# Kernel optimization log

Hardware: AMD Instinct MI355X
Metric: run time of the kernel (lower is better)

The kernel has to match this reference:

```python
import jax, jax.numpy as jnp
import numpy as np

HIDDEN = 768
KV_DIM = HIDDEN // 3  # 256
BATCH, SEQ = 2, 8192
THETA = 10000.0


def rope_table(seq_len, dim):
    # Matches LlamaRotaryEmbedding: returns [1, seq_len, dim] sinusoid table
    pos = jnp.arange(seq_len, dtype=jnp.float32)                       # [S]
    freqs = THETA ** (-jnp.arange(0, dim, 2, dtype=jnp.float32) / dim)  # [dim/2]
    ang = pos[:, None] * freqs[None, :]                                 # [S, dim/2]
    return jnp.concatenate([jnp.sin(ang), jnp.cos(ang)], axis=-1)[None]  # [1, S, dim]


def setup_inputs() -> dict:
    key = jax.random.key(0)
    kx, kq, kk, kv, ko = jax.random.split(key, 5)
    s = 1.0 / np.sqrt(HIDDEN)
    return {
        "x": jax.random.normal(kx, (BATCH, SEQ, HIDDEN), dtype=jnp.float32),
        # torch nn.Linear weights: [out_features, in_features], y = x @ W.T
        "Wq": jax.random.uniform(kq, (HIDDEN, HIDDEN), jnp.float32, -s, s),
        "Wk": jax.random.uniform(kk, (KV_DIM, HIDDEN), jnp.float32, -s, s),
        "Wv": jax.random.uniform(kv, (KV_DIM, HIDDEN), jnp.float32, -s, s),
        "Wo": jax.random.uniform(ko, (HIDDEN, KV_DIM), jnp.float32, -s, s),
    }


def reference(x, Wq, Wk, Wv, Wo):
    B, S, H = x.shape
    # q/k projections are computed in the original but immediately OVERWRITTEN
    # by the rope table (the rope module ignores its input values). Kept here
    # for faithfulness; XLA will DCE them in forward.
    q = jnp.einsum('bsh,oh->bso', x, Wq)
    k = jnp.einsum('bsh,oh->bso', x, Wk)
    v = jnp.einsum('bsh,oh->bso', x, Wv)                # [B, S, KV_DIM]
    r = rope_table(S, H)                                 # [1, S, H] -> q == k == r
    attn_weights = jnp.matmul(r, jnp.swapaxes(r, -2, -1))  # [1, S, S]
    attn_probs = jax.nn.softmax(attn_weights, axis=-1)      # [1, S, S]
    attn_output = jnp.matmul(attn_probs, v)                 # broadcast -> [B, S, KV_DIM]
    out = jnp.einsum('bsk,ok->bso', attn_output, Wo)        # [B, S, H]
    return out
```

## Files before the change

### kernel.cpp

```cpp
#include <hip/hip_runtime.h>


typedef unsigned short u16;
typedef __attribute__((ext_vector_type(8))) short short8;
typedef __attribute__((ext_vector_type(4))) float float4v;

__device__ inline u16 f32_to_bf16(float f) {
  union { float f; unsigned int u; } v; v.f = f;
  unsigned int r = v.u + 0x7FFF + ((v.u >> 16) & 1);
  return (u16)(r >> 16);
}

__global__ __launch_bounds__(256)
void prep_weights(const float* __restrict__ Wv, const float* __restrict__ Wo,
                  u16* __restrict__ wvt, u16* __restrict__ wot) {
  int id = blockIdx.x * 256 + threadIdx.x;
  union { u16 h[4]; uint2 u; } p;
  if (id < 49152) {
    int e = id * 4, n = e / 768, k = e - n * 768;
    float4v v = *(const float4v*)(Wv + (size_t)n * 768 + k);
    p.h[0] = f32_to_bf16(v[0]); p.h[1] = f32_to_bf16(v[1]);
    p.h[2] = f32_to_bf16(v[2]); p.h[3] = f32_to_bf16(v[3]);
    int t = k >> 5, kk = k & 31;
    *(uint2*)(wvt + ((t * 256 + n) * 32 + kk)) = p.u;
  } else {
    int e = (id - 49152) * 4, n = e / 256, k = e - n * 256;
    float4v v = *(const float4v*)(Wo + (size_t)n * 256 + k);
    p.h[0] = f32_to_bf16(v[0]); p.h[1] = f32_to_bf16(v[1]);
    p.h[2] = f32_to_bf16(v[2]); p.h[3] = f32_to_bf16(v[3]);
    int t = k >> 5, kk = k & 31;
    *(uint2*)(wot + ((t * 768 + n) * 32 + kk)) = p.u;
  }
}

template <bool WS>
__global__ __launch_bounds__(512, 1)
void fused_mfma(const float* __restrict__ x,
                const float* __restrict__ Wv, const float* __restrict__ Wo,
                const u16* __restrict__ wvt, const u16* __restrict__ wot,
                float* __restrict__ out) {
  __shared__ __align__(16) u16 As[64 * 32];
  __shared__ __align__(16) u16 Bs[256 * 32];
  __shared__ __align__(16) u16 Vs[64 * 264];

  const int tid = threadIdx.x;
  const int w  = tid >> 6, l = tid & 63;
  const int q  = l >> 4, mr = l & 15;
  const int wm = w & 1, wn = w >> 1;
  const int row0 = blockIdx.x * 64;

  const int xr = tid >> 3, xg = (tid & 7) * 4;
  const int wr = tid >> 1, wh = (tid & 1) * 16;

  float4v acc[2][4];
#pragma unroll
  for (int i = 0; i < 2; ++i)
#pragma unroll
    for (int j = 0; j < 4; ++j) acc[i][j] = (float4v){0.f, 0.f, 0.f, 0.f};

  for (int kt = 0; kt < 24; ++kt) {
    const int k0 = kt * 32;
    {
      float4v v = *(const float4v*)(x + (size_t)(row0 + xr) * 768 + k0 + xg);
      union { u16 h[4]; uint2 u; } p;
      p.h[0] = f32_to_bf16(v[0]); p.h[1] = f32_to_bf16(v[1]);
      p.h[2] = f32_to_bf16(v[2]); p.h[3] = f32_to_bf16(v[3]);
      *(uint2*)(As + xr * 32 + xg) = p.u;
    }
    if (WS) {
      const u16* g = wvt + (size_t)kt * (256 * 32);
#pragma unroll
      for (int p = 0; p < 2; ++p) {
        int c = tid + p * 512;
        *(short8*)(Bs + c * 8) = *(const short8*)(g + c * 8);
      }
    } else {
      const float* g = Wv + (size_t)wr * 768 + k0 + wh;
      union { u16 h[16]; short8 s[2]; } p;
#pragma unroll
      for (int u = 0; u < 4; ++u) {
        float4v v = *(const float4v*)(g + u * 4);
        p.h[u * 4 + 0] = f32_to_bf16(v[0]); p.h[u * 4 + 1] = f32_to_bf16(v[1]);
        p.h[u * 4 + 2] = f32_to_bf16(v[2]); p.h[u * 4 + 3] = f32_to_bf16(v[3]);
      }
      *(short8*)(Bs + wr * 32 + wh) = p.s[0];
      *(short8*)(Bs + wr * 32 + wh + 8) = p.s[1];
    }
    __syncthreads();

    short8 a[2], b[4];
#pragma unroll
    for (int i = 0; i < 2; ++i)
      a[i] = *(const short8*)(As + (wm * 32 + i * 16 + mr) * 32 + q * 8);
#pragma unroll
    for (int j = 0; j < 4; ++j)
      b[j] = *(const short8*)(Bs + (wn * 64 + j * 16 + mr) * 32 + q * 8);
#pragma unroll
    for (int i = 0; i < 2; ++i)
#pragma unroll
      for (int j = 0; j < 4; ++j)
        acc[i][j] = __builtin_amdgcn_mfma_f32_16x16x32_bf16(a[i], b[j], acc[i][j], 0, 0, 0);
    __syncthreads();
  }

#pragma unroll
  for (int i = 0; i < 2; ++i)
#pragma unroll
    for (int j = 0; j < 4; ++j) {
      int row = wm * 32 + i * 16 + q * 4;
      int col = wn * 64 + j * 16 + mr;
#pragma unroll
      for (int r = 0; r < 4; ++r)
        Vs[(row + r) * 264 + col] = f32_to_bf16(acc[i][j][r]);
    }
  __syncthreads();

  for (int c = 0; c < 3; ++c) {
    float4v acc2[2][4];
#pragma unroll
    for (int i = 0; i < 2; ++i)
#pragma unroll
      for (int j = 0; j < 4; ++j) acc2[i][j] = (float4v){0.f, 0.f, 0.f, 0.f};

    for (int kt = 0; kt < 8; ++kt) {
      const int k0 = kt * 32;
      if (WS) {
        const u16* g = wot + ((size_t)kt * 768 + c * 256) * 32;
#pragma unroll
        for (int p = 0; p < 2; ++p) {
          int cc = tid + p * 512;
          *(short8*)(Bs + cc * 8) = *(const short8*)(g + cc * 8);
        }
      } else {
        const float* g = Wo + (size_t)(c * 256 + wr) * 256 + k0 + wh;
        union { u16 h[16]; short8 s[2]; } p;
#pragma unroll
        for (int u = 0; u < 4; ++u) {
          float4v v = *(const float4v*)(g + u * 4);
          p.h[u * 4 + 0] = f32_to_bf16(v[0]); p.h[u * 4 + 1] = f32_to_bf16(v[1]);
          p.h[u * 4 + 2] = f32_to_bf16(v[2]); p.h[u * 4 + 3] = f32_to_bf16(v[3]);
        }
        *(short8*)(Bs + wr * 32 + wh) = p.s[0];
        *(short8*)(Bs + wr * 32 + wh + 8) = p.s[1];
      }
      __syncthreads();

      short8 a[2], b[4];
#pragma unroll
      for (int i = 0; i < 2; ++i)
        a[i] = *(const short8*)(Vs + (wm * 32 + i * 16 + mr) * 264 + k0 + q * 8);
#pragma unroll
      for (int j = 0; j < 4; ++j)
        b[j] = *(const short8*)(Bs + (wn * 64 + j * 16 + mr) * 32 + q * 8);
#pragma unroll
      for (int i = 0; i < 2; ++i)
#pragma unroll
        for (int j = 0; j < 4; ++j)
          acc2[i][j] = __builtin_amdgcn_mfma_f32_16x16x32_bf16(a[i], b[j], acc2[i][j], 0, 0, 0);
      __syncthreads();
    }

#pragma unroll
    for (int i = 0; i < 2; ++i)
#pragma unroll
      for (int j = 0; j < 4; ++j) {
        int row = row0 + wm * 32 + i * 16 + q * 4;
        int col = c * 256 + wn * 64 + j * 16 + mr;
#pragma unroll
        for (int r = 0; r < 4; ++r)
          out[(size_t)(row + r) * 768 + col] = acc2[i][j][r];
      }
  }
}

extern "C" void kernel_launch(void* const* d_in, const int* in_sizes, int n_in,
                              void* d_out, int out_size, void* d_ws, size_t ws_size,
                              hipStream_t stream) {
  (void)in_sizes; (void)n_in; (void)out_size;
  const float* x  = (const float*)d_in[0];
  const float* Wv = (const float*)d_in[3];
  const float* Wo = (const float*)d_in[4];
  float* out = (float*)d_out;

  if (ws_size >= 786432) {
    u16* wvt = (u16*)d_ws;
    u16* wot = wvt + 196608;
    prep_weights<<<dim3(384), dim3(256), 0, stream>>>(Wv, Wo, wvt, wot);
    fused_mfma<true><<<dim3(256), dim3(512), 0, stream>>>(x, Wv, Wo, wvt, wot, out);
  } else {
    fused_mfma<false><<<dim3(256), dim3(512), 0, stream>>>(x, Wv, Wo, nullptr, nullptr, out);
  }
}
```

Measured before the change: 136.4 us.

## Rewrite fused kernel with full-row LDS staging, register-direct fp16 weights, software pipelining

Replaces the two-kernel bf16 path with one fused kernel. It stages the full 64x768 x tile in swizzled LDS as fp16 and streams fp32 weights straight from global into registers, converting them to fp16 on the fly. A double-buffered K loop with s_setprio wraps the MFMAs, and per-K-step __syncthreads are dropped. Removing the prep kernel and the LDS weight tiles cuts barriers and a launch, at the cost of redundant global weight reads per wave, fp16 range/precision risk, and large LDS use (~128KB) that may limit occupancy.

Measured after the change: 148.0 us. +8.5%, slower.

```diff
diff --git a/kernel.cpp b/kernel.cpp
--- a/kernel.cpp
+++ b/kernel.cpp
@@ -3,191 +3,187 @@
 
 typedef unsigned short u16;
 typedef __attribute__((ext_vector_type(8))) short short8;
+typedef __attribute__((ext_vector_type(8))) _Float16 f16x8;
 typedef __attribute__((ext_vector_type(4))) float float4v;
 
-__device__ inline u16 f32_to_bf16(float f) {
-  union { float f; unsigned int u; } v; v.f = f;
-  unsigned int r = v.u + 0x7FFF + ((v.u >> 16) & 1);
-  return (u16)(r >> 16);
+__device__ inline u16 f16b(float f) {
+  union { _Float16 h; u16 u; } v; v.h = (_Float16)f; return v.u;
 }
 
-__global__ __launch_bounds__(256)
-void prep_weights(const float* __restrict__ Wv, const float* __restrict__ Wo,
-                  u16* __restrict__ wvt, u16* __restrict__ wot) {
-  int id = blockIdx.x * 256 + threadIdx.x;
-  union { u16 h[4]; uint2 u; } p;
-  if (id < 49152) {
-    int e = id * 4, n = e / 768, k = e - n * 768;
-    float4v v = *(const float4v*)(Wv + (size_t)n * 768 + k);
-    p.h[0] = f32_to_bf16(v[0]); p.h[1] = f32_to_bf16(v[1]);
-    p.h[2] = f32_to_bf16(v[2]); p.h[3] = f32_to_bf16(v[3]);
-    int t = k >> 5, kk = k & 31;
-    *(uint2*)(wvt + ((t * 256 + n) * 32 + kk)) = p.u;
-  } else {
-    int e = (id - 49152) * 4, n = e / 256, k = e - n * 256;
-    float4v v = *(const float4v*)(Wo + (size_t)n * 256 + k);
-    p.h[0] = f32_to_bf16(v[0]); p.h[1] = f32_to_bf16(v[1]);
-    p.h[2] = f32_to_bf16(v[2]); p.h[3] = f32_to_bf16(v[3]);
-    int t = k >> 5, kk = k & 31;
-    *(uint2*)(wot + ((t * 768 + n) * 32 + kk)) = p.u;
-  }
+__device__ inline f16x8 cv8(float4v a, float4v b) {
+  f16x8 r;
+#pragma unroll
+  for (int e = 0; e < 4; ++e) { r[e] = (_Float16)a[e]; r[e + 4] = (_Float16)b[e]; }
+  return r;
 }
 
-template <bool WS>
-__global__ __launch_bounds__(512, 1)
-void fused_mfma(const float* __restrict__ x,
-                const float* __restrict__ Wv, const float* __restrict__ Wo,
-                const u16* __restrict__ wvt, const u16* __restrict__ wot,
-                float* __restrict__ out) {
-  __shared__ __align__(16) u16 As[64 * 32];
-  __shared__ __align__(16) u16 Bs[256 * 32];
-  __shared__ __align__(16) u16 Vs[64 * 264];
+__global__ __launch_bounds__(512, 2)
+void fused2(const float* __restrict__ x, const float* __restrict__ Wv,
+            const float* __restrict__ Wo, float* __restrict__ out) {
+  __shared__ __align__(16) u16 S[64 * 768];
+  __shared__ __align__(16) u16 VL[64 * 256];
 
   const int tid = threadIdx.x;
-  const int w  = tid >> 6, l = tid & 63;
-  const int q  = l >> 4, mr = l & 15;
-  const int wm = w & 1, wn = w >> 1;
+  const int w = tid >> 6, l = tid & 63;
+  const int q = l >> 4, mr = l & 15;
   const int row0 = blockIdx.x * 64;
+  const int akey = mr & 7;
 
-  const int xr = tid >> 3, xg = (tid & 7) * 4;
-  const int wr = tid >> 1, wh = (tid & 1) * 16;
+  {
+    const int sr = ((w & 3) << 4) + mr;
+    const int half = w >> 2;
+    const float* gr = x + (size_t)(row0 + sr) * 768;
+    u16* lr = S + sr * 768;
+    const int key = sr & 7;
+#pragma unroll
+    for (int j = 0; j < 12; ++j) {
+      const int c = q + 4 * (2 * j + half);
+      float4v v0 = *(const float4v*)(gr + c * 8);
+      float4v v1 = *(const float4v*)(gr + c * 8 + 4);
+      union { u16 h[8]; short8 s; } p;
+#pragma unroll
+      for (int e = 0; e < 4; ++e) { p.h[e] = f16b(v0[e]); p.h[e + 4] = f16b(v1[e]); }
+      *(short8*)(lr + ((c ^ key) << 3)) = p.s;
+    }
+  }
+  __syncthreads();
 
-  float4v acc[2][4];
+  {
+    float4v acc1[4][2];
 #pragma unroll
-  for (int i = 0; i < 2; ++i)
+    for (int i = 0; i < 4; ++i)
 #pragma unroll
-    for (int j = 0; j < 4; ++j) acc[i][j] = (float4v){0.f, 0.f, 0.f, 0.f};
+      for (int j = 0; j < 2; ++j) acc1[i][j] = (float4v){0.f, 0.f, 0.f, 0.f};
 
-  for (int kt = 0; kt < 24; ++kt) {
-    const int k0 = kt * 32;
-    {
-      float4v v = *(const float4v*)(x + (size_t)(row0 + xr) * 768 + k0 + xg);
-      union { u16 h[4]; uint2 u; } p;
-      p.h[0] = f32_to_bf16(v[0]); p.h[1] = f32_to_bf16(v[1]);
-      p.h[2] = f32_to_bf16(v[2]); p.h[3] = f32_to_bf16(v[3]);
-      *(uint2*)(As + xr * 32 + xg) = p.u;
+    f16x8 a0[4], a1[4];
+    float4v e0a, e0b, e1a, e1b, o0a, o0b, o1a, o1b;
+
+#define LDA1(av_, kt_)                                                       \
+    _Pragma("unroll")                                                        \
+    for (int im = 0; im < 4; ++im)                                           \
+      av_[im] = *(const f16x8*)(                                             \
+          &S[(im * 16 + mr) * 768 + ((((kt_) * 4 + q) ^ akey) << 3)]);
+
+#define LDB1(s0a_, s0b_, s1a_, s1b_, kt_)                                    \
+    { const float* p0 = Wv + (size_t)(w * 32 + mr) * 768 + (kt_) * 32 + q * 8; \
+      const float* p1 = p0 + 16 * 768;                                       \
+      s0a_ = *(const float4v*)p0; s0b_ = *(const float4v*)(p0 + 4);          \
+      s1a_ = *(const float4v*)p1; s1b_ = *(const float4v*)(p1 + 4); }
+
+#define MM1(av_, s0a_, s0b_, s1a_, s1b_)                                     \
+    { f16x8 bf0 = cv8(s0a_, s0b_), bf1 = cv8(s1a_, s1b_);                    \
+      __builtin_amdgcn_s_setprio(1);                                         \
+      _Pragma("unroll")                                                      \
+      for (int im = 0; im < 4; ++im) {                                       \
+        acc1[im][0] = __builtin_amdgcn_mfma_f32_16x16x32_f16(av_[im], bf0, acc1[im][0], 0, 0, 0); \
+        acc1[im][1] = __builtin_amdgcn_mfma_f32_16x16x32_f16(av_[im], bf1, acc1[im][1], 0, 0, 0); \
+      }                                                                      \
+      __builtin_amdgcn_s_setprio(0); }
+
+    LDB1(e0a, e0b, e1a, e1b, 0)
+    LDA1(a0, 0)
+    for (int kt = 0; kt < 22; kt += 2) {
+      LDB1(o0a, o0b, o1a, o1b, kt + 1) LDA1(a1, kt + 1)
+      MM1(a0, e0a, e0b, e1a, e1b)
+      LDB1(e0a, e0b, e1a, e1b, kt + 2) LDA1(a0, kt + 2)
+      MM1(a1, o0a, o0b, o1a, o1b)
     }
-    if (WS) {
-      const u16* g = wvt + (size_t)kt * (256 * 32);
+    LDB1(o0a, o0b, o1a, o1b, 23) LDA1(a1, 23)
+    MM1(a0, e0a, e0b, e1a, e1b)
+    MM1(a1, o0a, o0b, o1a, o1b)
+
+#undef LDA1
+#undef LDB1
+#undef MM1
+
 #pragma unroll
-      for (int p = 0; p < 2; ++p) {
-        int c = tid + p * 512;
-        *(short8*)(Bs + c * 8) = *(const short8*)(g + c * 8);
+    for (int im = 0; im < 4; ++im)
+#pragma unroll
+      for (int jn = 0; jn < 2; ++jn) {
+        const int col = w * 32 + jn * 16 + mr;
+        const int cc = col >> 3, ce = col & 7;
+#pragma unroll
+        for (int r = 0; r < 4; ++r) {
+          const int rr = im * 16 + q * 4 + r;
+          VL[rr * 256 + ((cc ^ (rr & 7)) << 3) + ce] = f16b(acc1[im][jn][r]);
+        }
       }
-    } else {
-      const float* g = Wv + (size_t)wr * 768 + k0 + wh;
-      union { u16 h[16]; short8 s[2]; } p;
+  }
+  __syncthreads();
+
+  float4v acc2[4][6];
 #pragma unroll
-      for (int u = 0; u < 4; ++u) {
-        float4v v = *(const float4v*)(g + u * 4);
-        p.h[u * 4 + 0] = f32_to_bf16(v[0]); p.h[u * 4 + 1] = f32_to_bf16(v[1]);
-        p.h[u * 4 + 2] = f32_to_bf16(v[2]); p.h[u * 4 + 3] = f32_to_bf16(v[3]);
-      }
-      *(short8*)(Bs + wr * 32 + wh) = p.s[0];
-      *(short8*)(Bs + wr * 32 + wh + 8) = p.s[1];
+  for (int i = 0; i < 4; ++i)
+#pragma unroll
+    for (int j = 0; j < 6; ++j) acc2[i][j] = (float4v){0.f, 0.f, 0.f, 0.f};
+
+  {
+    f16x8 c0[4], c1[4];
+    float4v ge[6][2], go[6][2];
+
+#define LDA2(av_, kt_)                                                       \
+    _Pragma("unroll")                                                        \
+    for (int im = 0; im < 4; ++im)                                           \
+      av_[im] = *(const f16x8*)(                                             \
+          &VL[(im * 16 + mr) * 256 + ((((kt_) * 4 + q) ^ akey) << 3)]);
+
+#define LDB2(bv_, kt_)                                                       \
+    _Pragma("unroll")                                                        \
+    for (int jn = 0; jn < 6; ++jn) {                                         \
+      const float* p = Wo + (size_t)(w * 96 + jn * 16 + mr) * 256 + (kt_) * 32 + q * 8; \
+      bv_[jn][0] = *(const float4v*)p;                                       \
+      bv_[jn][1] = *(const float4v*)(p + 4);                                 \
     }
-    __syncthreads();
 
-    short8 a[2], b[4];
-#pragma unroll
-    for (int i = 0; i < 2; ++i)
-      a[i] = *(const short8*)(As + (wm * 32 + i * 16 + mr) * 32 + q * 8);
-#pragma unroll
-    for (int j = 0; j < 4; ++j)
-      b[j] = *(const short8*)(Bs + (wn * 64 + j * 16 + mr) * 32 + q * 8);
-#pragma unroll
-    for (int i = 0; i < 2; ++i)
-#pragma unroll
-      for (int j = 0; j < 4; ++j)
-        acc[i][j] = __builtin_amdgcn_mfma_f32_16x16x32_bf16(a[i], b[j], acc[i][j], 0, 0, 0);
-    __syncthreads();
+#define MM2(av_, bv_)                                                        \
+    { __builtin_amdgcn_s_setprio(1);                                         \
+      _Pragma("unroll")                                                      \
+      for (int jn = 0; jn < 6; ++jn) {                                       \
+        f16x8 bf = cv8(bv_[jn][0], bv_[jn][1]);                              \
+        _Pragma("unroll")                                                    \
+        for (int im = 0; im < 4; ++im)                                       \
+          acc2[im][jn] = __builtin_amdgcn_mfma_f32_16x16x32_f16(av_[im], bf, acc2[im][jn], 0, 0, 0); \
+      }                                                                      \
+      __builtin_amdgcn_s_setprio(0); }
+
+    LDB2(ge, 0)
+    LDA2(c0, 0)
+    for (int kt = 0; kt < 6; kt += 2) {
+      LDB2(go, kt + 1) LDA2(c1, kt + 1)
+      MM2(c0, ge)
+      LDB2(ge, kt + 2) LDA2(c0, kt + 2)
+      MM2(c1, go)
+    }
+    LDB2(go, 7) LDA2(c1, 7)
+    MM2(c0, ge)
+    MM2(c1, go)
+
+#undef LDA2
+#undef LDB2
+#undef MM2
   }
 
 #pragma unroll
-  for (int i = 0; i < 2; ++i)
+  for (int im = 0; im < 4; ++im)
 #pragma unroll
-    for (int j = 0; j < 4; ++j) {
-      int row = wm * 32 + i * 16 + q * 4;
-      int col = wn * 64 + j * 16 + mr;
+    for (int jn = 0; jn < 6; ++jn) {
+      const int r0 = row0 + im * 16 + q * 4;
+      const int c  = w * 96 + jn * 16 + mr;
 #pragma unroll
       for (int r = 0; r < 4; ++r)
-        Vs[(row + r) * 264 + col] = f32_to_bf16(acc[i][j][r]);
+        out[(size_t)(r0 + r) * 768 + c] = acc2[im][jn][r];
     }
-  __syncthreads();
-
-  for (int c = 0; c < 3; ++c) {
-    float4v acc2[2][4];
-#pragma unroll
-    for (int i = 0; i < 2; ++i)
-#pragma unroll
-      for (int j = 0; j < 4; ++j) acc2[i][j] = (float4v){0.f, 0.f, 0.f, 0.f};
-
-    for (int kt = 0; kt < 8; ++kt) {
-      const int k0 = kt * 32;
-      if (WS) {
-        const u16* g = wot + ((size_t)kt * 768 + c * 256) * 32;
-#pragma unroll
-        for (int p = 0; p < 2; ++p) {
-          int cc = tid + p * 512;
-          *(short8*)(Bs + cc * 8) = *(const short8*)(g + cc * 8);
-        }
-      } else {
-        const float* g = Wo + (size_t)(c * 256 + wr) * 256 + k0 + wh;
-        union { u16 h[16]; short8 s[2]; } p;
-#pragma unroll
-        for (int u = 0; u < 4; ++u) {
-          float4v v = *(const float4v*)(g + u * 4);
-          p.h[u * 4 + 0] = f32_to_bf16(v[0]); p.h[u * 4 + 1] = f32_to_bf16(v[1]);
-          p.h[u * 4 + 2] = f32_to_bf16(v[2]); p.h[u * 4 + 3] = f32_to_bf16(v[3]);
-        }
-        *(short8*)(Bs + wr * 32 + wh) = p.s[0];
-        *(short8*)(Bs + wr * 32 + wh + 8) = p.s[1];
-      }
-      __syncthreads();
-
-      short8 a[2], b[4];
-#pragma unroll
-      for (int i = 0; i < 2; ++i)
-        a[i] = *(const short8*)(Vs + (wm * 32 + i * 16 + mr) * 264 + k0 + q * 8);
-#pragma unroll
-      for (int j = 0; j < 4; ++j)
-        b[j] = *(const short8*)(Bs + (wn * 64 + j * 16 + mr) * 32 + q * 8);
-#pragma unroll
-      for (int i = 0; i < 2; ++i)
-#pragma unroll
-        for (int j = 0; j < 4; ++j)
-          acc2[i][j] = __builtin_amdgcn_mfma_f32_16x16x32_bf16(a[i], b[j], acc2[i][j], 0, 0, 0);
-      __syncthreads();
-    }
-
-#pragma unroll
-    for (int i = 0; i < 2; ++i)
-#pragma unroll
-      for (int j = 0; j < 4; ++j) {
-        int row = row0 + wm * 32 + i * 16 + q * 4;
-        int col = c * 256 + wn * 64 + j * 16 + mr;
-#pragma unroll
-        for (int r = 0; r < 4; ++r)
-          out[(size_t)(row + r) * 768 + col] = acc2[i][j][r];
-      }
-  }
 }
 
 extern "C" void kernel_launch(void* const* d_in, const int* in_sizes, int n_in,
                               void* d_out, int out_size, void* d_ws, size_t ws_size,
                               hipStream_t stream) {
   (void)in_sizes; (void)n_in; (void)out_size;
+  (void)d_ws; (void)ws_size;
   const float* x  = (const float*)d_in[0];
   const float* Wv = (const float*)d_in[3];
   const float* Wo = (const float*)d_in[4];
   float* out = (float*)d_out;
 
-  if (ws_size >= 786432) {
-    u16* wvt = (u16*)d_ws;
-    u16* wot = wvt + 196608;
-    prep_weights<<<dim3(384), dim3(256), 0, stream>>>(Wv, Wo, wvt, wot);
-    fused_mfma<true><<<dim3(256), dim3(512), 0, stream>>>(x, Wv, Wo, wvt, wot, out);
-  } else {
-    fused_mfma<false><<<dim3(256), dim3(512), 0, stream>>>(x, Wv, Wo, nullptr, nullptr, out);
-  }
+  fused2<<<dim3(256), dim3(512), 0, stream>>>(x, Wv, Wo, out);
 }
```
